# Optimization experiments

Measured on AMD Instinct MI355X. Metric: run time of the kernel, lower is better.

Reference implementation:

```python
import jax, jax.numpy as jnp
import numpy as np

DIM = 128
POS_HID = 64
ATTN_HID = DIM * 4
K_NEIGH = 16


def _mlp2(x, w1, b1, w2, b2):
    # Linear -> ReLU -> Linear (weights stored as (in, out))
    return jax.nn.relu(x @ w1 + b1) @ w2 + b2


def setup_inputs() -> dict:
    key = jax.random.key(0)
    ks = jax.random.split(key, 12)
    B, N = 2, 512
    s = 0.05
    return {
        "x": jax.random.normal(ks[0], (B, DIM, N), jnp.float32),
        "pos": jax.random.normal(ks[1], (B, N, 3), jnp.float32),
        "w_qkv": jax.random.normal(ks[2], (DIM, 3 * DIM), jnp.float32) * s,
        "pos_w1": jax.random.normal(ks[3], (3, POS_HID), jnp.float32) * s,
        "pos_b1": jnp.zeros((POS_HID,), jnp.float32),
        "pos_w2": jax.random.normal(ks[4], (POS_HID, DIM), jnp.float32) * s,
        "pos_b2": jnp.zeros((DIM,), jnp.float32),
        "attn_w1": jax.random.normal(ks[5], (DIM, ATTN_HID), jnp.float32) * s,
        "attn_b1": jnp.zeros((ATTN_HID,), jnp.float32),
        "attn_w2": jax.random.normal(ks[6], (ATTN_HID, DIM), jnp.float32) * s,
        "attn_b2": jnp.zeros((DIM,), jnp.float32),
    }


def reference(x, pos, w_qkv, pos_w1, pos_b1, pos_w2, pos_b2,
              attn_w1, attn_b1, attn_w2, attn_b2):
    # x: (B, dim, N) -> (B, N, dim)
    xt = jnp.swapaxes(x, 1, 2)
    B, N, d = xt.shape

    qkv = xt @ w_qkv                           # (B, N, 3d), no bias
    q, k, v = jnp.split(qkv, 3, axis=-1)

    rel_pos = pos[:, :, None, :] - pos[:, None, :, :]          # (B, N, N, 3)
    rel_pos_emb = _mlp2(rel_pos, pos_w1, pos_b1, pos_w2, pos_b2)  # (B, N, N, d)
    qk_rel = q[:, :, None, :] - k[:, None, :, :]               # (B, N, N, d)

    # KNN: smallest euclidean rel distances per query point
    rel_dist = jnp.sqrt(jnp.sum(rel_pos * rel_pos, axis=-1))   # (B, N, N)
    _, idx = jax.lax.top_k(-rel_dist, K_NEIGH)                 # (B, N, K)

    idxe = idx[..., None]                                      # (B, N, K, 1)
    v_g = v[jnp.arange(B)[:, None, None], idx]                 # (B, N, K, d)
    qk_g = jnp.take_along_axis(qk_rel, idxe, axis=2)           # (B, N, K, d)
    pe_g = jnp.take_along_axis(rel_pos_emb, idxe, axis=2)      # (B, N, K, d)

    v_g = v_g + pe_g
    sim = _mlp2(qk_g + pe_g, attn_w1, attn_b1, attn_w2, attn_b2)  # (B, N, K, d)
    attn = jax.nn.softmax(sim, axis=-2)                        # softmax over neighbors
    agg = jnp.einsum('bikd,bikd->bid', attn, v_g)              # (B, N, d)
    return jnp.swapaxes(agg, 1, 2)                             # (B, d, N)
```

## Files before the change

### kernel.cpp

```cpp
#include <hip/hip_runtime.h>
#include <math.h>

#define DIM 128
#define N_PTS 512
#define K_NEIGH 16
#define POS_HID 64
#define ATTN_HID 512

typedef __attribute__((ext_vector_type(8))) short short8;
typedef __attribute__((ext_vector_type(4))) float f32x4;
typedef unsigned short us;
typedef unsigned long long ull;

__device__ __forceinline__ us f2b(float f) {
    unsigned int u = __builtin_bit_cast(unsigned int, f);
    u += 0x7fffu + ((u >> 16) & 1u);
    return (us)(u >> 16);
}

__device__ __forceinline__ ull shflx64(ull v, int m) {
    int lo = __shfl_xor((int)(unsigned int)v, m);
    int hi = __shfl_xor((int)(unsigned int)(v >> 32), m);
    return ((ull)(unsigned int)hi << 32) | (unsigned int)lo;
}

__global__ __launch_bounds__(256)
void qkv_pack_kernel(const float* __restrict__ x,
                     const float* __restrict__ wqkv,
                     const float* __restrict__ aw1,
                     const float* __restrict__ aw2,
                     const float* __restrict__ pw2,
                     float* __restrict__ qkv,
                     us* __restrict__ p1, us* __restrict__ p2,
                     us* __restrict__ p3, int npts) {
    __shared__ __align__(16) us xA[16][136];
    const int tid = threadIdx.x;
    const int nq = npts >> 2;

    if ((int)blockIdx.x >= nq) {
        int t = ((int)blockIdx.x - nq) * 256 + tid;
        if (t < 65536) {
            int j = t & 7, l = (t >> 3) & 63, nt = (t >> 9) & 31, ks = t >> 14;
            int k = ks * 32 + (l >> 4) * 8 + j, n = nt * 16 + (l & 15);
            p1[t] = f2b(aw1[k * ATTN_HID + n]);
        } else if (t < 131072) {
            int u = t - 65536;
            int j = u & 7, l = (u >> 3) & 63, nt = (u >> 9) & 7, ch = u >> 12;
            int k = ch * 32 + (l >> 4) * 8 + j, n = nt * 16 + (l & 15);
            p2[u] = f2b(aw2[k * DIM + n]);
        } else if (t < 139264) {
            int u = t - 131072;
            int j = u & 7, l = (u >> 3) & 63, nt = (u >> 9) & 7, ks = u >> 12;
            int k = ks * 32 + (l >> 4) * 8 + j, n = nt * 16 + (l & 15);
            p3[u] = f2b(pw2[k * DIM + n]);
        }
        return;
    }

    const int w = tid >> 6, lane = tid & 63, quad = lane >> 4, lq = lane & 15;
    const int n0 = ((int)blockIdx.x >> 2) * 16;
    const int ntb = ((int)blockIdx.x & 3) * 6;
    const int b = n0 >> 9, nn = n0 & (N_PTS - 1);
#pragma unroll
    for (int rr = 0; rr < 8; ++rr) {
        int id = rr * 256 + tid;
        int d = id >> 4, i = id & 15;
        xA[i][d] = f2b(x[(size_t)(b * DIM + d) * N_PTS + nn + i]);
    }
    __syncthreads();
    short8 a[4];
#pragma unroll
    for (int ks = 0; ks < 4; ++ks)
        a[ks] = *(const short8*)&xA[lq][ks * 32 + quad * 8];
#pragma unroll
    for (int i = 0; i < 2; ++i) {
        int nl = w + i * 4;
        if (nl < 6) {
            int nt = ntb + nl;
            f32x4 acc = {0.f, 0.f, 0.f, 0.f};
#pragma unroll
            for (int ks = 0; ks < 4; ++ks) {
                const float* wp = wqkv + (size_t)(ks * 32 + quad * 8) * 384 + nt * 16 + lq;
                short8 bf;
#pragma unroll
                for (int j = 0; j < 8; ++j) bf[j] = (short)f2b(wp[(size_t)j * 384]);
                acc = __builtin_amdgcn_mfma_f32_16x16x32_bf16(a[ks], bf, acc, 0, 0, 0);
            }
#pragma unroll
            for (int r = 0; r < 4; ++r)
                qkv[(size_t)(n0 + quad * 4 + r) * 384 + nt * 16 + lq] = acc[r];
        }
    }
}

__global__ __launch_bounds__(256, 1)
void attn_fused_kernel(const float* __restrict__ pos,
                       const float* __restrict__ qkv,
                       const float* __restrict__ pw1,
                       const float* __restrict__ pb1,
                       const float* __restrict__ pb2,
                       const us* __restrict__ p1,
                       const us* __restrict__ p2,
                       const us* __restrict__ p3,
                       const float* __restrict__ ab1,
                       float* __restrict__ out) {
    __shared__ __align__(16) us hinA[4][16][136];
    __shared__ __align__(16) us h1s[4][2][16][40];
    __shared__ int nbrs[4][16];

    const int tid = threadIdx.x;
    const int w = tid >> 6, lane = tid & 63, quad = lane >> 4, lq = lane & 15;
    const int g = blockIdx.x * 4 + w, b = g >> 9, n = g & (N_PTS - 1);

    short8 b3f[2][8];
#pragma unroll
    for (int ks = 0; ks < 2; ++ks)
#pragma unroll
        for (int nt = 0; nt < 8; ++nt)
            b3f[ks][nt] = *(const short8*)(p3 + (size_t)((ks * 8 + nt) * 64 + lane) * 8);

    float w1x[2][8], w1y[2][8], w1z[2][8], w1b[2][8];
#pragma unroll
    for (int ks = 0; ks < 2; ++ks)
#pragma unroll
        for (int jj = 0; jj < 8; ++jj) {
            int c = ks * 32 + quad * 8 + jj;
            w1x[ks][jj] = pw1[c];
            w1y[ks][jj] = pw1[64 + c];
            w1z[ks][jj] = pw1[128 + c];
            w1b[ks][jj] = pb1[c];
        }

    float qvr[8], pb2r[8], ab1r[32];
#pragma unroll
    for (int nt = 0; nt < 8; ++nt) {
        qvr[nt]  = qkv[(size_t)g * 384 + nt * 16 + lq];
        pb2r[nt] = pb2[nt * 16 + lq];
    }
#pragma unroll
    for (int nt = 0; nt < 32; ++nt) ab1r[nt] = ab1[nt * 16 + lq];

    {
        const float pix = pos[g * 3 + 0], piy = pos[g * 3 + 1], piz = pos[g * 3 + 2];
        float d2[8];
#pragma unroll
        for (int rr = 0; rr < 8; ++rr) {
            int j = rr * 64 + lane;
            float dx = pix - pos[(b * N_PTS + j) * 3 + 0];
            float dy = piy - pos[(b * N_PTS + j) * 3 + 1];
            float dz = piz - pos[(b * N_PTS + j) * 3 + 2];
            d2[rr] = dx * dx + dy * dy + dz * dz;
        }
        for (int r = 0; r < K_NEIGH; ++r) {
            ull key = ~0ULL;
#pragma unroll
            for (int rr = 0; rr < 8; ++rr) {
                unsigned int fb = __builtin_bit_cast(unsigned int, d2[rr]);
                ull k2 = ((ull)fb << 32) | (unsigned int)(rr * 64 + lane);
                key = k2 < key ? k2 : key;
            }
#pragma unroll
            for (int off = 32; off > 0; off >>= 1) {
                ull o = shflx64(key, off);
                key = o < key ? o : key;
            }
            unsigned int jw = (unsigned int)key;
            if (lane == 0) nbrs[w][r] = (int)jw;
            if (lane == (int)(jw & 63)) d2[jw >> 6] = __builtin_inff();
        }
    }

    short8 pha[2];
    {
        const int jn = nbrs[w][lq];
        float rx = pos[g * 3 + 0] - pos[(b * N_PTS + jn) * 3 + 0];
        float ry = pos[g * 3 + 1] - pos[(b * N_PTS + jn) * 3 + 1];
        float rz = pos[g * 3 + 2] - pos[(b * N_PTS + jn) * 3 + 2];
#pragma unroll
        for (int ks = 0; ks < 2; ++ks) {
            short8 f;
#pragma unroll
            for (int jj = 0; jj < 8; ++jj) {
                float h = rx * w1x[ks][jj] + ry * w1y[ks][jj] + rz * w1z[ks][jj] + w1b[ks][jj];
                f[jj] = (short)f2b(fmaxf(h, 0.f));
            }
            pha[ks] = f;
        }
    }

    f32x4 pe[8];
#pragma unroll
    for (int nt = 0; nt < 8; ++nt) {
        f32x4 acc = {0.f, 0.f, 0.f, 0.f};
        acc = __builtin_amdgcn_mfma_f32_16x16x32_bf16(pha[0], b3f[0][nt], acc, 0, 0, 0);
        acc = __builtin_amdgcn_mfma_f32_16x16x32_bf16(pha[1], b3f[1][nt], acc, 0, 0, 0);
#pragma unroll
        for (int r = 0; r < 4; ++r) pe[nt][r] = acc[r] + pb2r[nt];
    }

    f32x4 vg[8];
    {
        int jr[4];
#pragma unroll
        for (int r = 0; r < 4; ++r) jr[r] = nbrs[w][quad * 4 + r];
#pragma unroll
        for (int nt = 0; nt < 8; ++nt) {
            int d = nt * 16 + lq;
#pragma unroll
            for (int r = 0; r < 4; ++r) {
                const float* kv = qkv + (size_t)(b * N_PTS + jr[r]) * 384;
                float pp = pe[nt][r];
                hinA[w][quad * 4 + r][d] = f2b(qvr[nt] - kv[128 + d] + pp);
                vg[nt][r] = kv[256 + d] + pp;
            }
        }
    }

    short8 a1f[4];
#pragma unroll
    for (int ks = 0; ks < 4; ++ks)
        a1f[ks] = *(const short8*)&hinA[w][lq][ks * 32 + quad * 8];

    f32x4 c2[8];
#pragma unroll
    for (int nt = 0; nt < 8; ++nt) c2[nt] = (f32x4){0.f, 0.f, 0.f, 0.f};

    short8 p1f[2][2][4];
    short8 p2f[2][8];

#pragma unroll
    for (int t = 0; t < 2; ++t)
#pragma unroll
        for (int ks = 0; ks < 4; ++ks)
            p1f[0][t][ks] = *(const short8*)(p1 + (size_t)(((ks << 5) + t) * 64 + lane) * 8);
#pragma unroll
    for (int nt2 = 0; nt2 < 8; ++nt2)
        p2f[0][nt2] = *(const short8*)(p2 + (size_t)(nt2 * 64 + lane) * 8);
#pragma unroll
    for (int t = 0; t < 2; ++t) {
        f32x4 acc = {0.f, 0.f, 0.f, 0.f};
#pragma unroll
        for (int ks = 0; ks < 4; ++ks)
            acc = __builtin_amdgcn_mfma_f32_16x16x32_bf16(a1f[ks], p1f[0][t][ks], acc, 0, 0, 0);
        float bias = ab1r[t];
#pragma unroll
        for (int r = 0; r < 4; ++r)
            h1s[w][0][quad * 4 + r][t * 16 + lq] = f2b(fmaxf(acc[r] + bias, 0.f));
    }
#pragma unroll
    for (int t = 0; t < 2; ++t)
#pragma unroll
        for (int ks = 0; ks < 4; ++ks)
            p1f[1][t][ks] = *(const short8*)(p1 + (size_t)(((ks << 5) + 2 + t) * 64 + lane) * 8);

#pragma unroll
    for (int ch = 0; ch < 16; ++ch) {
        const int cb = ch & 1, nb = cb ^ 1;
        const short8 a2 = *(const short8*)&h1s[w][cb][lq][quad * 8];
        if (ch < 14) {
#pragma unroll
            for (int t = 0; t < 2; ++t)
#pragma unroll
                for (int ks = 0; ks < 4; ++ks)
                    p1f[cb][t][ks] = *(const short8*)(p1 + (size_t)(((ks << 5) + (ch + 2) * 2 + t) * 64 + lane) * 8);
        }
        if (ch < 15) {
#pragma unroll
            for (int nt2 = 0; nt2 < 8; ++nt2)
                p2f[nb][nt2] = *(const short8*)(p2 + (size_t)((((ch + 1) << 3) + nt2) * 64 + lane) * 8);
        }
        if (ch < 15) {
#pragma unroll
            for (int t = 0; t < 2; ++t) {
                int nt = (ch + 1) * 2 + t;
                f32x4 acc = {0.f, 0.f, 0.f, 0.f};
#pragma unroll
                for (int ks = 0; ks < 4; ++ks)
                    acc = __builtin_amdgcn_mfma_f32_16x16x32_bf16(a1f[ks], p1f[nb][t][ks], acc, 0, 0, 0);
                float bias = ab1r[nt];
#pragma unroll
                for (int r = 0; r < 4; ++r)
                    h1s[w][nb][quad * 4 + r][t * 16 + lq] = f2b(fmaxf(acc[r] + bias, 0.f));
            }
        }
#pragma unroll
        for (int nt2 = 0; nt2 < 8; ++nt2)
            c2[nt2] = __builtin_amdgcn_mfma_f32_16x16x32_bf16(a2, p2f[cb][nt2], c2[nt2], 0, 0, 0);
    }

#pragma unroll
    for (int nt2 = 0; nt2 < 8; ++nt2) {
        f32x4 s4 = c2[nt2];
        float m = fmaxf(fmaxf(s4[0], s4[1]), fmaxf(s4[2], s4[3]));
        m = fmaxf(m, __shfl_xor(m, 16));
        m = fmaxf(m, __shfl_xor(m, 32));
        float e0 = __expf(s4[0] - m), e1 = __expf(s4[1] - m);
        float e2 = __expf(s4[2] - m), e3 = __expf(s4[3] - m);
        float s = e0 + e1 + e2 + e3;
        f32x4 v4 = vg[nt2];
        float a = e0 * v4[0] + e1 * v4[1] + e2 * v4[2] + e3 * v4[3];
        s += __shfl_xor(s, 16); s += __shfl_xor(s, 32);
        a += __shfl_xor(a, 16); a += __shfl_xor(a, 32);
        if (quad == 0)
            out[(size_t)(b * DIM + nt2 * 16 + lq) * N_PTS + n] = a / s;
    }
}

extern "C" void kernel_launch(void* const* d_in, const int* in_sizes, int n_in,
                              void* d_out, int out_size, void* d_ws, size_t ws_size,
                              hipStream_t stream) {
    const float* x    = (const float*)d_in[0];
    const float* pos  = (const float*)d_in[1];
    const float* wqkv = (const float*)d_in[2];
    const float* pw1  = (const float*)d_in[3];
    const float* pb1  = (const float*)d_in[4];
    const float* pw2  = (const float*)d_in[5];
    const float* pb2  = (const float*)d_in[6];
    const float* aw1  = (const float*)d_in[7];
    const float* ab1  = (const float*)d_in[8];
    const float* aw2  = (const float*)d_in[9];
    float* out = (float*)d_out;

    int B = in_sizes[0] / (DIM * N_PTS);
    int npts = B * N_PTS;

    char* ws = (char*)d_ws;
    float* qkv = (float*)ws;
    us* p1 = (us*)(ws + (size_t)npts * 384 * 4);
    us* p2 = p1 + 65536;
    us* p3 = p2 + 65536;

    int nq = npts / 4;
    int grid = nq + (139264 + 255) / 256;
    qkv_pack_kernel<<<grid, 256, 0, stream>>>(x, wqkv, aw1, aw2, pw2,
                                              qkv, p1, p2, p3, npts);
    attn_fused_kernel<<<npts / 4, 256, 0, stream>>>(pos, qkv,
                                                    pw1, pb1, pb2,
                                                    p1, p2, p3, ab1, out);
}
```

Before: 99.14 us.

## Stage attention MLP weights through shared LDS double buffer across waves

Instead of every wave loading its own copy of the attn MLP weight fragments from global memory into registers, the four waves in a block now cooperatively load each chunk once into a double-buffered LDS region and read MFMA operands from LDS. This cuts global/L2 weight traffic by four and frees registers, but adds a block-wide __syncthreads per chunk and LDS read traffic, and removes the cross-chunk register-level overlap of layer-1 with layer-2.

```diff
diff --git a/kernel.cpp b/kernel.cpp
--- a/kernel.cpp
+++ b/kernel.cpp
@@ -105,12 +105,16 @@
                        const float* __restrict__ ab1,
                        float* __restrict__ out) {
     __shared__ __align__(16) us hinA[4][16][136];
-    __shared__ __align__(16) us h1s[4][2][16][40];
+    __shared__ __align__(16) us h1s[4][16][40];
     __shared__ int nbrs[4][16];
+    __shared__ __align__(16) us wbuf[2][8192];
 
     const int tid = threadIdx.x;
     const int w = tid >> 6, lane = tid & 63, quad = lane >> 4, lq = lane & 15;
     const int g = blockIdx.x * 4 + w, b = g >> 9, n = g & (N_PTS - 1);
+    const int f0 = w, f1 = 4 + w;
+    const size_t p1o0 = (size_t)(((f0 >> 1) << 5) + (f0 & 1)) * 512 + lane * 8;
+    const size_t p1o1 = (size_t)(((f1 >> 1) << 5) + (f1 & 1)) * 512 + lane * 8;
 
     short8 b3f[2][8];
 #pragma unroll
@@ -225,67 +229,55 @@
 #pragma unroll
     for (int nt = 0; nt < 8; ++nt) c2[nt] = (f32x4){0.f, 0.f, 0.f, 0.f};
 
-    short8 p1f[2][2][4];
-    short8 p2f[2][8];
-
-#pragma unroll
-    for (int t = 0; t < 2; ++t)
-#pragma unroll
-        for (int ks = 0; ks < 4; ++ks)
-            p1f[0][t][ks] = *(const short8*)(p1 + (size_t)(((ks << 5) + t) * 64 + lane) * 8);
-#pragma unroll
-    for (int nt2 = 0; nt2 < 8; ++nt2)
-        p2f[0][nt2] = *(const short8*)(p2 + (size_t)(nt2 * 64 + lane) * 8);
-#pragma unroll
-    for (int t = 0; t < 2; ++t) {
-        f32x4 acc = {0.f, 0.f, 0.f, 0.f};
-#pragma unroll
-        for (int ks = 0; ks < 4; ++ks)
-            acc = __builtin_amdgcn_mfma_f32_16x16x32_bf16(a1f[ks], p1f[0][t][ks], acc, 0, 0, 0);
-        float bias = ab1r[t];
-#pragma unroll
-        for (int r = 0; r < 4; ++r)
-            h1s[w][0][quad * 4 + r][t * 16 + lq] = f2b(fmaxf(acc[r] + bias, 0.f));
-    }
-#pragma unroll
-    for (int t = 0; t < 2; ++t)
-#pragma unroll
-        for (int ks = 0; ks < 4; ++ks)
-            p1f[1][t][ks] = *(const short8*)(p1 + (size_t)(((ks << 5) + 2 + t) * 64 + lane) * 8);
+    {
+        short8 s0 = *(const short8*)(p1 + p1o0);
+        short8 s1 = *(const short8*)(p1 + p1o1);
+        short8 s2 = *(const short8*)(p2 + (size_t)tid * 8);
+        short8 s3 = *(const short8*)(p2 + 2048 + (size_t)tid * 8);
+        *(short8*)&wbuf[0][f0 * 512 + lane * 8] = s0;
+        *(short8*)&wbuf[0][f1 * 512 + lane * 8] = s1;
+        *(short8*)&wbuf[0][4096 + tid * 8] = s2;
+        *(short8*)&wbuf[0][4096 + 2048 + tid * 8] = s3;
+    }
+    __syncthreads();
 
 #pragma unroll
     for (int ch = 0; ch < 16; ++ch) {
         const int cb = ch & 1, nb = cb ^ 1;
-        const short8 a2 = *(const short8*)&h1s[w][cb][lq][quad * 8];
-        if (ch < 14) {
-#pragma unroll
-            for (int t = 0; t < 2; ++t)
-#pragma unroll
-                for (int ks = 0; ks < 4; ++ks)
-                    p1f[cb][t][ks] = *(const short8*)(p1 + (size_t)(((ks << 5) + (ch + 2) * 2 + t) * 64 + lane) * 8);
-        }
+        short8 s0, s1, s2, s3;
         if (ch < 15) {
-#pragma unroll
-            for (int nt2 = 0; nt2 < 8; ++nt2)
-                p2f[nb][nt2] = *(const short8*)(p2 + (size_t)((((ch + 1) << 3) + nt2) * 64 + lane) * 8);
+            const int cc = ch + 1;
+            s0 = *(const short8*)(p1 + (size_t)cc * 1024 + p1o0);
+            s1 = *(const short8*)(p1 + (size_t)cc * 1024 + p1o1);
+            s2 = *(const short8*)(p2 + (size_t)cc * 4096 + tid * 8);
+            s3 = *(const short8*)(p2 + (size_t)cc * 4096 + 2048 + tid * 8);
+        }
+#pragma unroll
+        for (int t = 0; t < 2; ++t) {
+            f32x4 acc = {0.f, 0.f, 0.f, 0.f};
+#pragma unroll
+            for (int ks = 0; ks < 4; ++ks) {
+                const short8 wf = *(const short8*)&wbuf[cb][((ks << 1) + t) * 512 + lane * 8];
+                acc = __builtin_amdgcn_mfma_f32_16x16x32_bf16(a1f[ks], wf, acc, 0, 0, 0);
+            }
+            float bias = ab1r[ch * 2 + t];
+#pragma unroll
+            for (int r = 0; r < 4; ++r)
+                h1s[w][quad * 4 + r][t * 16 + lq] = f2b(fmaxf(acc[r] + bias, 0.f));
+        }
+        const short8 a2 = *(const short8*)&h1s[w][lq][quad * 8];
+#pragma unroll
+        for (int nt2 = 0; nt2 < 8; ++nt2) {
+            const short8 wf = *(const short8*)&wbuf[cb][4096 + nt2 * 512 + lane * 8];
+            c2[nt2] = __builtin_amdgcn_mfma_f32_16x16x32_bf16(a2, wf, c2[nt2], 0, 0, 0);
         }
         if (ch < 15) {
-#pragma unroll
-            for (int t = 0; t < 2; ++t) {
-                int nt = (ch + 1) * 2 + t;
-                f32x4 acc = {0.f, 0.f, 0.f, 0.f};
-#pragma unroll
-                for (int ks = 0; ks < 4; ++ks)
-                    acc = __builtin_amdgcn_mfma_f32_16x16x32_bf16(a1f[ks], p1f[nb][t][ks], acc, 0, 0, 0);
-                float bias = ab1r[nt];
-#pragma unroll
-                for (int r = 0; r < 4; ++r)
-                    h1s[w][nb][quad * 4 + r][t * 16 + lq] = f2b(fmaxf(acc[r] + bias, 0.f));
-            }
-        }
-#pragma unroll
-        for (int nt2 = 0; nt2 < 8; ++nt2)
-            c2[nt2] = __builtin_amdgcn_mfma_f32_16x16x32_bf16(a2, p2f[cb][nt2], c2[nt2], 0, 0, 0);
+            *(short8*)&wbuf[nb][f0 * 512 + lane * 8] = s0;
+            *(short8*)&wbuf[nb][f1 * 512 + lane * 8] = s1;
+            *(short8*)&wbuf[nb][4096 + tid * 8] = s2;
+            *(short8*)&wbuf[nb][4096 + 2048 + tid * 8] = s3;
+        }
+        __syncthreads();
     }
 
 #pragma unroll
```

Result: slower. 108.0 us (+8.9%).
